# Performance work log

Hardware: AMD Instinct MI355X
Metric: run time of the kernel (lower is better)

The kernel has to match this reference:

```python
import jax, jax.numpy as jnp
import numpy as np

N, E = 20000, 320000
NODE_DIM, EDGE_DIM, EMB, HEADS, HIDDEN, OUT = 128, 16, 128, 4, 512, 64
NEG_SLOPE = 0.2


def _gatv2(x, src0, dst0, ea, Wl, bl, Wr, br, We, att, bias):
    """PyG GATv2Conv (concat=True, add_self_loops=True, fill_value='mean')."""
    n = x.shape[0]
    e = src0.shape[0]
    H, C = att.shape
    # self loops; self-loop edge_attr = mean of incoming edge_attr per node (0 if none)
    cnt = jax.ops.segment_sum(jnp.ones((e,), x.dtype), dst0, num_segments=n)
    loop_attr = jax.ops.segment_sum(ea, dst0, num_segments=n) / jnp.maximum(cnt, 1.0)[:, None]
    loops = jnp.arange(n, dtype=src0.dtype)
    src = jnp.concatenate([src0, loops])
    dst = jnp.concatenate([dst0, loops])
    ea_full = jnp.concatenate([ea, loop_attr], axis=0)
    xl = (x @ Wl + bl).reshape(n, H, C)   # source transform
    xr = (x @ Wr + br).reshape(n, H, C)   # target transform
    ef = (ea_full @ We).reshape(-1, H, C)  # edge transform (no bias in PyG)
    s = jax.nn.leaky_relu(xl[src] + xr[dst] + ef, NEG_SLOPE)  # [E', H, C]
    logits = jnp.einsum('ehc,hc->eh', s, att)
    # scatter-softmax over incoming edges of each dst node (stable)
    mx = jax.ops.segment_max(logits, dst, num_segments=n)
    num = jnp.exp(logits - mx[dst])
    den = jax.ops.segment_sum(num, dst, num_segments=n)
    alpha = num / (den[dst] + 1e-16)
    out = jax.ops.segment_sum(alpha[:, :, None] * xl[src], dst, num_segments=n)
    return out.reshape(n, H * C) + bias


def _lin(key, fan_in, fan_out, dt=jnp.float32):
    return jax.random.normal(key, (fan_in, fan_out), dt) * (1.0 / np.sqrt(fan_in))


def setup_inputs() -> dict:
    key = jax.random.key(0)
    ks = jax.random.split(key, 24)
    HC = HEADS * EMB
    inp = {
        'x': jax.random.normal(ks[0], (N, NODE_DIM), jnp.float32),
        'edge_index': jax.random.randint(ks[1], (2, E), 0, N, jnp.int64),
        'edge_attr': jax.random.normal(ks[2], (E, EDGE_DIM), jnp.float32),
        # GATv2 layer 1
        'Wl1': _lin(ks[3], NODE_DIM, HC), 'bl1': jnp.zeros((HC,), jnp.float32),
        'Wr1': _lin(ks[4], NODE_DIM, HC), 'br1': jnp.zeros((HC,), jnp.float32),
        'We1': _lin(ks[5], EDGE_DIM, HC),
        'att1': jax.random.normal(ks[6], (HEADS, EMB), jnp.float32) * (1.0 / np.sqrt(EMB)),
        'bias1': jnp.zeros((HC,), jnp.float32),
        # GATv2 layer 2
        'Wl2': _lin(ks[7], HC, HC), 'bl2': jnp.zeros((HC,), jnp.float32),
        'Wr2': _lin(ks[8], HC, HC), 'br2': jnp.zeros((HC,), jnp.float32),
        'We2': _lin(ks[9], EDGE_DIM, HC),
        'att2': jax.random.normal(ks[10], (HEADS, EMB), jnp.float32) * (1.0 / np.sqrt(EMB)),
        'bias2': jnp.zeros((HC,), jnp.float32),
        # decoder MLP
        'Wd1': _lin(ks[11], HC, HIDDEN), 'bd1': jnp.zeros((HIDDEN,), jnp.float32),
        'Wd2': _lin(ks[12], HIDDEN, OUT), 'bd2': jnp.zeros((OUT,), jnp.float32),
    }
    return inp


def reference(x, edge_index, edge_attr,
              Wl1, bl1, Wr1, br1, We1, att1, bias1,
              Wl2, bl2, Wr2, br2, We2, att2, bias2,
              Wd1, bd1, Wd2, bd2):
    src, dst = edge_index[0], edge_index[1]
    h = _gatv2(x, src, dst, edge_attr, Wl1, bl1, Wr1, br1, We1, att1, bias1)
    h = _gatv2(h, src, dst, edge_attr, Wl2, bl2, Wr2, br2, We2, att2, bias2)
    q = jax.nn.relu(h @ Wd1 + bd1) @ Wd2 + bd2
    return q
```

## Files before the change

### kernel.cpp

```cpp
#include <hip/hip_runtime.h>
#include <hip/hip_fp16.h>

typedef _Float16 half8 __attribute__((ext_vector_type(8)));
typedef _Float16 half2v __attribute__((ext_vector_type(2)));
typedef float f32x4 __attribute__((ext_vector_type(4)));

#if __has_builtin(__builtin_amdgcn_fdot2)
#define FDOT2(a, b, c) __builtin_amdgcn_fdot2((a), (b), (c), false)
#else
static __device__ __forceinline__ float FDOT2(half2v a, half2v b, float c) {
  return (float)a[0] * (float)b[0] + (float)a[1] * (float)b[1] + c;
}
#endif
#define H2(v8, p) ((half2v){(v8)[2 * (p)], (v8)[2 * (p) + 1]})

#define GLOAD_LDS16(gp, lp)                                                        \
  __builtin_amdgcn_global_load_lds(                                                \
      (const __attribute__((address_space(1))) void*)(gp),                         \
      (__attribute__((address_space(3))) void*)(lp), 16, 0, 0)

template <int CTRL>
__device__ __forceinline__ float dpp_add16(float x) {
  int y = __builtin_amdgcn_update_dpp(0, __float_as_int(x), CTRL, 0xf, 0xf, true);
  return x + __int_as_float(y);
}
__device__ __forceinline__ float rowsum16(float x) {
  x = dpp_add16<0x128>(x);
  x = dpp_add16<0x124>(x);
  x = dpp_add16<0x122>(x);
  x = dpp_add16<0x121>(x);
  return x;
}

__global__ void prep_kernel(const float* __restrict__ x, _Float16* __restrict__ x16, int nx,
                            const float* __restrict__ Wl1, const float* __restrict__ Wr1,
                            _Float16* __restrict__ WlrT1,
                            const float* __restrict__ Wl2, const float* __restrict__ Wr2,
                            _Float16* __restrict__ WlrT2,
                            const float* __restrict__ Wd1, _Float16* __restrict__ WdT1,
                            const float* __restrict__ Wd2, _Float16* __restrict__ WdT2,
                            const float* __restrict__ We1, _Float16* __restrict__ WeK1,
                            const float* __restrict__ We2, _Float16* __restrict__ WeK2,
                            const float* __restrict__ att1, _Float16* __restrict__ att16_1,
                            const float* __restrict__ att2, _Float16* __restrict__ att16_2,
                            const int* __restrict__ dst0, int* __restrict__ deg, int E) {
  int i = blockIdx.x * 256 + threadIdx.x;
  if (i < nx) { x16[i] = (_Float16)x[i]; return; }
  i -= nx;
  if (i < 1024 * 128) {
    int n = i >> 7, k = i & 127;
    float v = (n < 512) ? Wl1[(size_t)k * 512 + n] : Wr1[(size_t)k * 512 + (n - 512)];
    WlrT1[i] = (_Float16)v; return;
  }
  i -= 1024 * 128;
  if (i < 1024 * 512) {
    int n = i >> 9, k = i & 511;
    float v = (n < 512) ? Wl2[(size_t)k * 512 + n] : Wr2[(size_t)k * 512 + (n - 512)];
    WlrT2[i] = (_Float16)v; return;
  }
  i -= 1024 * 512;
  if (i < 512 * 512) { int n = i >> 9, k = i & 511; WdT1[i] = (_Float16)Wd1[(size_t)k * 512 + n]; return; }
  i -= 512 * 512;
  if (i < 64 * 512)  { int n = i >> 9, k = i & 511; WdT2[i] = (_Float16)Wd2[(size_t)k * 64 + n]; return; }
  i -= 64 * 512;
  if (i < 512 * 16)  { WeK1[i] = (_Float16)We1[i]; return; }
  i -= 512 * 16;
  if (i < 512 * 16)  { WeK2[i] = (_Float16)We2[i]; return; }
  i -= 512 * 16;
  if (i < 512)       { att16_1[i] = (_Float16)att1[i]; return; }
  i -= 512;
  if (i < 512)       { att16_2[i] = (_Float16)att2[i]; return; }
  i -= 512;
  if (i < E)         { atomicAdd(&deg[dst0[i]], 1); return; }
}

__global__ __launch_bounds__(1024) void scan_kernel(const int* __restrict__ deg, int* __restrict__ offs, int N) {
  __shared__ int part[1024];
  int t = threadIdx.x;
  int chunk = (N + 1023) / 1024;
  int b = t * chunk, e = min(b + chunk, N);
  int s = 0;
  for (int i = b; i < e; i++) s += deg[i] + 1;
  part[t] = s;
  __syncthreads();
  for (int off = 1; off < 1024; off <<= 1) {
    int v = (t >= off) ? part[t - off] : 0;
    __syncthreads();
    part[t] += v;
    __syncthreads();
  }
  int run = (t == 0) ? 0 : part[t - 1];
  for (int i = b; i < e; i++) { offs[i] = run; run += deg[i] + 1; }
  if (t == 1023) offs[N] = part[1023];
}

__global__ void csr_fill_kernel(const int* __restrict__ src0, const int* __restrict__ dst0,
                                const float* __restrict__ ea,
                                const int* __restrict__ offs, const int* __restrict__ deg,
                                int* __restrict__ cnt, int* __restrict__ csr_src,
                                _Float16* __restrict__ eas, int E, int N) {
  int i = blockIdx.x * 256 + threadIdx.x;
  if (i < 16) {
    csr_src[E + N + i] = 0;
#pragma unroll
    for (int k = 0; k < 16; k++) eas[(size_t)(E + N + i) * 16 + k] = (_Float16)0.f;
  }
  if (i < E) {
    int d = dst0[i];
    int p = offs[d] + atomicAdd(&cnt[d], 1);
    csr_src[p] = src0[i];
    const float* s = ea + (size_t)i * 16;
    half8 h0, h1;
#pragma unroll
    for (int k = 0; k < 8; k++) { h0[k] = (_Float16)s[k]; h1[k] = (_Float16)s[k + 8]; }
    *(half8*)(eas + (size_t)p * 16) = h0;
    *(half8*)(eas + (size_t)p * 16 + 8) = h1;
  } else if (i < E + N) {
    int v = i - E;
    csr_src[offs[v] + deg[v]] = v;
  }
}

__global__ void loop_attr_kernel(const int* __restrict__ offs, const int* __restrict__ deg,
                                 _Float16* __restrict__ eas, int N) {
  int i = blockIdx.x * 256 + threadIdx.x;
  if (i >= N * 16) return;
  int v = i >> 4, k = i & 15;
  int b = offs[v], dg = deg[v];
  float s = 0.f;
  for (int j = 0; j < dg; j++) s += (float)eas[((size_t)(b + j)) * 16 + k];
  eas[((size_t)(b + dg)) * 16 + k] = (_Float16)(s / fmaxf((float)dg, 1.0f));
}

template <bool RELU, bool OUT_F32>
__global__ __launch_bounds__(256) void gemm_f16(const _Float16* __restrict__ A,
                                                const _Float16* __restrict__ BT,
                                                const float* __restrict__ biasA,
                                                const float* __restrict__ biasB,
                                                void* __restrict__ C,
                                                int M, int K, int Nfull, int ldc) {
  __shared__ _Float16 As[128 * 32];
  __shared__ _Float16 Bs[128 * 32];
  int t = threadIdx.x;
  int m0 = blockIdx.x * 128;
  int n0 = blockIdx.y * 128;
  int l = t & 63, w = t >> 6;
  int wm = w & 1, wn = w >> 1;
  int lr = l & 15, lq = l >> 4;

  f32x4 acc[4][4];
#pragma unroll
  for (int i = 0; i < 4; i++)
#pragma unroll
    for (int j = 0; j < 4; j++) acc[i][j] = (f32x4){0.f, 0.f, 0.f, 0.f};

  int r0 = w * 32 + (l >> 2);
  int cb = (l & 3) * 8;
  const _Float16* Ap = A + (size_t)(m0 + r0) * K + cb;
  const _Float16* Bp = BT + (size_t)(n0 + r0) * K + cb;
  _Float16* AsW = As + w * 32 * 32;
  _Float16* BsW = Bs + w * 32 * 32;

  for (int kk = 0; kk < K; kk += 32) {
    GLOAD_LDS16(Ap, AsW);
    GLOAD_LDS16(Ap + (size_t)16 * K, AsW + 16 * 32);
    GLOAD_LDS16(Bp, BsW);
    GLOAD_LDS16(Bp + (size_t)16 * K, BsW + 16 * 32);
    Ap += 32; Bp += 32;
    __syncthreads();
    half8 af[4], bf[4];
#pragma unroll
    for (int mi = 0; mi < 4; mi++) af[mi] = *(const half8*)&As[(wm * 64 + mi * 16 + lr) * 32 + lq * 8];
#pragma unroll
    for (int ni = 0; ni < 4; ni++) bf[ni] = *(const half8*)&Bs[(wn * 64 + ni * 16 + lr) * 32 + lq * 8];
#pragma unroll
    for (int mi = 0; mi < 4; mi++)
#pragma unroll
      for (int ni = 0; ni < 4; ni++)
        acc[mi][ni] = __builtin_amdgcn_mfma_f32_16x16x32_f16(af[mi], bf[ni], acc[mi][ni], 0, 0, 0);
    __syncthreads();
  }

#pragma unroll
  for (int ni = 0; ni < 4; ni++) {
    int col = n0 + wn * 64 + ni * 16 + lr;
    if (col >= Nfull) continue;
    float bv = (col < 512) ? biasA[col] : biasB[col - 512];
#pragma unroll
    for (int mi = 0; mi < 4; mi++) {
#pragma unroll
      for (int r = 0; r < 4; r++) {
        int row = m0 + wm * 64 + mi * 16 + lq * 4 + r;
        if (row >= M) continue;
        float v = acc[mi][ni][r] + bv;
        if (RELU) v = fmaxf(v, 0.f);
        if (OUT_F32) ((float*)C)[(size_t)row * ldc + col] = v;
        else ((_Float16*)C)[(size_t)row * ldc + col] = (_Float16)v;
      }
    }
  }
}


__device__ __forceinline__ void upd(float p, half8 xs, float& m, float& den, float acc[8]) {
  float mn = fmaxf(m, p);
  float sc = __expf(m - mn);
  float al = __expf(p - mn);
  den = den * sc + al;
#pragma unroll
  for (int jj = 0; jj < 8; jj++) acc[jj] = acc[jj] * sc + al * (float)xs[jj];
  m = mn;
}

__global__ __launch_bounds__(256) void gat_fused_kernel(
    const _Float16* __restrict__ xlr,
    const int* __restrict__ csr_src, const int* __restrict__ offs,
    const _Float16* __restrict__ eas,
    const _Float16* __restrict__ WeK,
    const _Float16* __restrict__ att16,
    const float* __restrict__ bias,
    _Float16* __restrict__ hout, int N) {
  __shared__ _Float16 WeL[16 * 512];
  int t = threadIdx.x;
  int l = t & 63;
  int w = t >> 6;
  int h = l >> 4;
  int c0 = l * 8;

  {
    const _Float16* gW = WeK + w * 512 + l * 8;
    _Float16* lW = WeL + w * 512;
#pragma unroll
    for (int p = 0; p < 4; p++) GLOAD_LDS16(gW + p * 2048, lW + p * 2048);
  }
  __syncthreads();

  half8 attv = *(const half8*)(att16 + h * 128 + (l & 15) * 8);
  const half2v lk = {(_Float16)0.2f, (_Float16)0.2f};

  int wid = blockIdx.x * 4 + w;
  int nw = gridDim.x * 4;

  for (int v0 = wid; v0 < N; v0 += nw) {
    int v = __builtin_amdgcn_readfirstlane(v0);
    int b = offs[v], e2 = offs[v + 1];
    half8 xrv = *(const half8*)(xlr + (size_t)v * 1024 + 512 + c0);

    int s0 = csr_src[b], s1 = csr_src[b + 1], s2 = csr_src[b + 2], s3 = csr_src[b + 3];
    half8 xs0 = *(const half8*)(xlr + (size_t)s0 * 1024 + c0);
    half8 xs1 = *(const half8*)(xlr + (size_t)s1 * 1024 + c0);
    half8 xs2 = *(const half8*)(xlr + (size_t)s2 * 1024 + c0);
    half8 xs3 = *(const half8*)(xlr + (size_t)s3 * 1024 + c0);
    half8 a00 = *(const half8*)(eas + (size_t)b * 16);
    half8 a01 = *(const half8*)(eas + (size_t)b * 16 + 8);
    half8 a10 = *(const half8*)(eas + (size_t)(b + 1) * 16);
    half8 a11 = *(const half8*)(eas + (size_t)(b + 1) * 16 + 8);
    half8 a20 = *(const half8*)(eas + (size_t)(b + 2) * 16);
    half8 a21 = *(const half8*)(eas + (size_t)(b + 2) * 16 + 8);
    half8 a30 = *(const half8*)(eas + (size_t)(b + 3) * 16);
    half8 a31 = *(const half8*)(eas + (size_t)(b + 3) * 16 + 8);
    int t0 = csr_src[b + 4], t1 = csr_src[b + 5], t2 = csr_src[b + 6], t3 = csr_src[b + 7];

    float m = -1e30f, den = 0.f;
    float acc[8];
#pragma unroll
    for (int j = 0; j < 8; j++) acc[j] = 0.f;

    for (int j = b; j < e2; j += 4) {
      half8 nx0 = *(const half8*)(xlr + (size_t)t0 * 1024 + c0);
      half8 nx1 = *(const half8*)(xlr + (size_t)t1 * 1024 + c0);
      half8 nx2 = *(const half8*)(xlr + (size_t)t2 * 1024 + c0);
      half8 nx3 = *(const half8*)(xlr + (size_t)t3 * 1024 + c0);
      half8 n00 = *(const half8*)(eas + (size_t)(j + 4) * 16);
      half8 n01 = *(const half8*)(eas + (size_t)(j + 4) * 16 + 8);
      half8 n10 = *(const half8*)(eas + (size_t)(j + 5) * 16);
      half8 n11 = *(const half8*)(eas + (size_t)(j + 5) * 16 + 8);
      half8 n20 = *(const half8*)(eas + (size_t)(j + 6) * 16);
      half8 n21 = *(const half8*)(eas + (size_t)(j + 6) * 16 + 8);
      half8 n30 = *(const half8*)(eas + (size_t)(j + 7) * 16);
      half8 n31 = *(const half8*)(eas + (size_t)(j + 7) * 16 + 8);
      int u0 = csr_src[j + 8], u1 = csr_src[j + 9], u2 = csr_src[j + 10], u3 = csr_src[j + 11];

      half2v e0[4], e1[4], e2v[4], e3[4];
#pragma unroll
      for (int p = 0; p < 4; p++) {
        e0[p] = (half2v){0, 0}; e1[p] = (half2v){0, 0};
        e2v[p] = (half2v){0, 0}; e3[p] = (half2v){0, 0};
      }
#pragma unroll
      for (int k = 0; k < 16; k++) {
        half8 wr = *(const half8*)(WeL + k * 512 + c0);
        _Float16 q0 = (k < 8) ? a00[k] : a01[k - 8];
        _Float16 q1 = (k < 8) ? a10[k] : a11[k - 8];
        _Float16 q2 = (k < 8) ? a20[k] : a21[k - 8];
        _Float16 q3 = (k < 8) ? a30[k] : a31[k - 8];
        half2v k0 = {q0, q0}, k1 = {q1, q1}, k2 = {q2, q2}, k3 = {q3, q3};
#pragma unroll
        for (int p = 0; p < 4; p++) {
          half2v wp = H2(wr, p);
          e0[p] += k0 * wp;
          e1[p] += k1 * wp;
          e2v[p] += k2 * wp;
          e3[p] += k3 * wp;
        }
      }
      float p0 = 0.f, p1 = 0.f, p2 = 0.f, p3 = 0.f;
#pragma unroll
      for (int p = 0; p < 4; p++) {
        half2v xrp = H2(xrv, p);
        half2v ap = H2(attv, p);
        half2v v0 = H2(xs0, p) + xrp + e0[p];
        half2v v1 = H2(xs1, p) + xrp + e1[p];
        half2v v2 = H2(xs2, p) + xrp + e2v[p];
        half2v v3 = H2(xs3, p) + xrp + e3[p];
        v0 = __builtin_elementwise_max(v0, v0 * lk);
        v1 = __builtin_elementwise_max(v1, v1 * lk);
        v2 = __builtin_elementwise_max(v2, v2 * lk);
        v3 = __builtin_elementwise_max(v3, v3 * lk);
        p0 = FDOT2(v0, ap, p0);
        p1 = FDOT2(v1, ap, p1);
        p2 = FDOT2(v2, ap, p2);
        p3 = FDOT2(v3, ap, p3);
      }
      p0 = rowsum16(p0); p1 = rowsum16(p1); p2 = rowsum16(p2); p3 = rowsum16(p3);

      upd(p0, xs0, m, den, acc);
      if (j + 1 < e2) upd(p1, xs1, m, den, acc);
      if (j + 2 < e2) upd(p2, xs2, m, den, acc);
      if (j + 3 < e2) upd(p3, xs3, m, den, acc);

      xs0 = nx0; xs1 = nx1; xs2 = nx2; xs3 = nx3;
      a00 = n00; a01 = n01; a10 = n10; a11 = n11;
      a20 = n20; a21 = n21; a30 = n30; a31 = n31;
      t0 = u0; t1 = u1; t2 = u2; t3 = u3;
    }
    float rd = 1.f / (den + 1e-16f);
    half8 o;
#pragma unroll
    for (int jj = 0; jj < 8; jj++) o[jj] = (_Float16)(fmaf(acc[jj], rd, bias[c0 + jj]));
    *(half8*)(hout + (size_t)v * 512 + c0) = o;
  }
}


extern "C" void kernel_launch(void* const* d_in, const int* in_sizes, int n_in,
                              void* d_out, int out_size, void* d_ws, size_t ws_size,
                              hipStream_t stream) {
  (void)n_in; (void)out_size; (void)ws_size;
  const float* x    = (const float*)d_in[0];
  const int*   ei   = (const int*)d_in[1];
  const float* ea   = (const float*)d_in[2];
  const float* Wl1  = (const float*)d_in[3];
  const float* bl1  = (const float*)d_in[4];
  const float* Wr1  = (const float*)d_in[5];
  const float* br1  = (const float*)d_in[6];
  const float* We1  = (const float*)d_in[7];
  const float* att1 = (const float*)d_in[8];
  const float* bias1= (const float*)d_in[9];
  const float* Wl2  = (const float*)d_in[10];
  const float* bl2  = (const float*)d_in[11];
  const float* Wr2  = (const float*)d_in[12];
  const float* br2  = (const float*)d_in[13];
  const float* We2  = (const float*)d_in[14];
  const float* att2 = (const float*)d_in[15];
  const float* bias2= (const float*)d_in[16];
  const float* Wd1  = (const float*)d_in[17];
  const float* bd1  = (const float*)d_in[18];
  const float* Wd2  = (const float*)d_in[19];
  const float* bd2  = (const float*)d_in[20];

  const int N = in_sizes[0] / 128;
  const int E = in_sizes[1] / 2;
  const int EP = E + N;
  const int Npad = (N + 127) & ~127;
  const int* src0 = ei;
  const int* dst0 = ei + E;

  char* ws = (char*)d_ws;
  size_t off = 0;
  auto alloc = [&](size_t bytes) -> void* {
    void* p = ws + off;
    off += (bytes + 255) & ~(size_t)255;
    return p;
  };

  int*   deg    = (int*)alloc((size_t)N * 8);
  int*   cnt    = deg + N;
  int*   offs   = (int*)alloc(((size_t)N + 1) * 4);
  int*   csr_src= (int*)alloc(((size_t)EP + 16) * 4);
  _Float16* eas = (_Float16*)alloc(((size_t)EP + 16) * 16 * 2);
  _Float16* x16   = (_Float16*)alloc((size_t)Npad * 128 * 2);
  _Float16* xlr16 = (_Float16*)alloc((size_t)Npad * 1024 * 2);
  _Float16* h16   = (_Float16*)alloc((size_t)Npad * 512 * 2);
  _Float16* WlrT1 = (_Float16*)alloc(1024 * 128 * 2);
  _Float16* WlrT2 = (_Float16*)alloc(1024 * 512 * 2);
  _Float16* WdT1  = (_Float16*)alloc(512 * 512 * 2);
  _Float16* WdT2  = (_Float16*)alloc(128 * 512 * 2);
  _Float16* WeK1  = (_Float16*)alloc(16 * 512 * 2);
  _Float16* WeK2  = (_Float16*)alloc(16 * 512 * 2);
  _Float16* att16_1 = (_Float16*)alloc(512 * 2);
  _Float16* att16_2 = (_Float16*)alloc(512 * 2);
  _Float16* t16   = xlr16;

  hipMemsetAsync(deg, 0, (size_t)N * 8, stream);

  int nx = N * 128;
  int prep_base = nx + 1024 * 128 + 1024 * 512 + 512 * 512 + 64 * 512
                + 512 * 16 + 512 * 16 + 512 + 512;
  int prep_total = prep_base + E;
  prep_kernel<<<(prep_total + 255) / 256, 256, 0, stream>>>(
      x, x16, nx, Wl1, Wr1, WlrT1, Wl2, Wr2, WlrT2,
      Wd1, WdT1, Wd2, WdT2, We1, WeK1, We2, WeK2,
      att1, att16_1, att2, att16_2, dst0, deg, E);

  int g;
  scan_kernel<<<1, 1024, 0, stream>>>(deg, offs, N);
  g = (EP + 255) / 256;
  csr_fill_kernel<<<g, 256, 0, stream>>>(src0, dst0, ea, offs, deg, cnt, csr_src, eas, E, N);
  g = (N * 16 + 255) / 256;
  loop_attr_kernel<<<g, 256, 0, stream>>>(offs, deg, eas, N);

  dim3 gb(256);
  dim3 ggm((N + 127) / 128, 8);
  dim3 ggd((N + 127) / 128, 4);
  dim3 ggo((N + 127) / 128, 1);

  const int FGRID = 2048;

  gemm_f16<false, false><<<ggm, gb, 0, stream>>>(x16, WlrT1, bl1, br1, xlr16, N, 128, 1024, 1024);
  gat_fused_kernel<<<FGRID, 256, 0, stream>>>(xlr16, csr_src, offs, eas, WeK1, att16_1, bias1, h16, N);

  gemm_f16<false, false><<<ggm, gb, 0, stream>>>(h16, WlrT2, bl2, br2, xlr16, N, 512, 1024, 1024);
  gat_fused_kernel<<<FGRID, 256, 0, stream>>>(xlr16, csr_src, offs, eas, WeK2, att16_2, bias2, h16, N);

  gemm_f16<true, false><<<ggd, gb, 0, stream>>>(h16, WdT1, bd1, bd1, t16, N, 512, 512, 512);
  gemm_f16<false, true><<<ggo, gb, 0, stream>>>(t16, WdT2, bd2, bd2, d_out, N, 512, 64, 64);
}
```

Before: 534.1 us.

## Compute per-edge edge-feature projections with MFMA into swizzled LDS tiles

Inside the fused GAT kernel, the per-edge edge_attr @ We projection moves from packed-half FMAs per edge to 16x16x16 MFMA instructions. Each wave computes a chunk of 16 edges by 512 channels into a per-wave swizzled LDS buffer, and the attention loop reads those projections back from LDS. We is reordered in prep to suit the MFMA A-fragment layout, and padding is extended to cover chunk overreads. Separately, the loop-attr mean kernel uses one wave per node with shuffle reduction. The cost is 64KB of extra LDS per block, which may reduce occupancy, and wasted MFMA work for nodes with low degree.

```diff
diff --git a/kernel.cpp b/kernel.cpp
--- a/kernel.cpp
+++ b/kernel.cpp
@@ -2,6 +2,7 @@
 #include <hip/hip_fp16.h>
 
 typedef _Float16 half8 __attribute__((ext_vector_type(8)));
+typedef _Float16 half4 __attribute__((ext_vector_type(4)));
 typedef _Float16 half2v __attribute__((ext_vector_type(2)));
 typedef float f32x4 __attribute__((ext_vector_type(4)));
 
@@ -39,8 +40,8 @@
                             _Float16* __restrict__ WlrT2,
                             const float* __restrict__ Wd1, _Float16* __restrict__ WdT1,
                             const float* __restrict__ Wd2, _Float16* __restrict__ WdT2,
-                            const float* __restrict__ We1, _Float16* __restrict__ WeK1,
-                            const float* __restrict__ We2, _Float16* __restrict__ WeK2,
+                            const float* __restrict__ We1, _Float16* __restrict__ WeF1,
+                            const float* __restrict__ We2, _Float16* __restrict__ WeF2,
                             const float* __restrict__ att1, _Float16* __restrict__ att16_1,
                             const float* __restrict__ att2, _Float16* __restrict__ att16_2,
                             const int* __restrict__ dst0, int* __restrict__ deg, int E) {
@@ -63,9 +64,15 @@
   i -= 512 * 512;
   if (i < 64 * 512)  { int n = i >> 9, k = i & 511; WdT2[i] = (_Float16)Wd2[(size_t)k * 64 + n]; return; }
   i -= 64 * 512;
-  if (i < 512 * 16)  { WeK1[i] = (_Float16)We1[i]; return; }
+  if (i < 512 * 16) {
+    int k = i & 15, c = (i >> 4) & 15, g = i >> 8;
+    WeF1[i] = (_Float16)We1[(size_t)k * 512 + g * 16 + c]; return;
+  }
   i -= 512 * 16;
-  if (i < 512 * 16)  { WeK2[i] = (_Float16)We2[i]; return; }
+  if (i < 512 * 16) {
+    int k = i & 15, c = (i >> 4) & 15, g = i >> 8;
+    WeF2[i] = (_Float16)We2[(size_t)k * 512 + g * 16 + c]; return;
+  }
   i -= 512 * 16;
   if (i < 512)       { att16_1[i] = (_Float16)att1[i]; return; }
   i -= 512;
@@ -100,8 +107,8 @@
                                 int* __restrict__ cnt, int* __restrict__ csr_src,
                                 _Float16* __restrict__ eas, int E, int N) {
   int i = blockIdx.x * 256 + threadIdx.x;
-  if (i < 16) {
-    csr_src[E + N + i] = 0;
+  if (i < 64) {
+    if (i < 16) csr_src[E + N + i] = 0;
 #pragma unroll
     for (int k = 0; k < 16; k++) eas[(size_t)(E + N + i) * 16 + k] = (_Float16)0.f;
   }
@@ -123,13 +130,17 @@
 
 __global__ void loop_attr_kernel(const int* __restrict__ offs, const int* __restrict__ deg,
                                  _Float16* __restrict__ eas, int N) {
-  int i = blockIdx.x * 256 + threadIdx.x;
-  if (i >= N * 16) return;
-  int v = i >> 4, k = i & 15;
-  int b = offs[v], dg = deg[v];
+  int wid = (blockIdx.x * 256 + threadIdx.x) >> 6;
+  int l = threadIdx.x & 63;
+  if (wid >= N) return;
+  int b = offs[wid], dg = deg[wid];
+  int k = l & 15, r = l >> 4;
   float s = 0.f;
-  for (int j = 0; j < dg; j++) s += (float)eas[((size_t)(b + j)) * 16 + k];
-  eas[((size_t)(b + dg)) * 16 + k] = (_Float16)(s / fmaxf((float)dg, 1.0f));
+  for (int j = r; j < dg; j += 4)
+    s += (float)eas[(size_t)(b + j) * 16 + k];
+  s += __shfl_xor(s, 16, 64);
+  s += __shfl_xor(s, 32, 64);
+  if (r == 0) eas[(size_t)(b + dg) * 16 + k] = (_Float16)(s / fmaxf((float)dg, 1.0f));
 }
 
 template <bool RELU, bool OUT_F32>
@@ -216,26 +227,29 @@
     const _Float16* __restrict__ xlr,
     const int* __restrict__ csr_src, const int* __restrict__ offs,
     const _Float16* __restrict__ eas,
-    const _Float16* __restrict__ WeK,
+    const _Float16* __restrict__ WeF,
     const _Float16* __restrict__ att16,
     const float* __restrict__ bias,
     _Float16* __restrict__ hout, int N) {
-  __shared__ _Float16 WeL[16 * 512];
+  __shared__ _Float16 WeFL[16 * 512];
+  __shared__ _Float16 EFs[4][16 * 512];
   int t = threadIdx.x;
   int l = t & 63;
   int w = t >> 6;
   int h = l >> 4;
   int c0 = l * 8;
+  int lr = l & 15, lq = l >> 4;
 
   {
-    const _Float16* gW = WeK + w * 512 + l * 8;
-    _Float16* lW = WeL + w * 512;
+    const _Float16* gW = WeF + w * 512 + l * 8;
+    _Float16* lW = WeFL + w * 512;
 #pragma unroll
     for (int p = 0; p < 4; p++) GLOAD_LDS16(gW + p * 2048, lW + p * 2048);
   }
   __syncthreads();
 
-  half8 attv = *(const half8*)(att16 + h * 128 + (l & 15) * 8);
+  _Float16* EFw = &EFs[w][0];
+  half8 attv = *(const half8*)(att16 + h * 128 + lr * 8);
   const half2v lk = {(_Float16)0.2f, (_Float16)0.2f};
 
   int wid = blockIdx.x * 4 + w;
@@ -251,88 +265,67 @@
     half8 xs1 = *(const half8*)(xlr + (size_t)s1 * 1024 + c0);
     half8 xs2 = *(const half8*)(xlr + (size_t)s2 * 1024 + c0);
     half8 xs3 = *(const half8*)(xlr + (size_t)s3 * 1024 + c0);
-    half8 a00 = *(const half8*)(eas + (size_t)b * 16);
-    half8 a01 = *(const half8*)(eas + (size_t)b * 16 + 8);
-    half8 a10 = *(const half8*)(eas + (size_t)(b + 1) * 16);
-    half8 a11 = *(const half8*)(eas + (size_t)(b + 1) * 16 + 8);
-    half8 a20 = *(const half8*)(eas + (size_t)(b + 2) * 16);
-    half8 a21 = *(const half8*)(eas + (size_t)(b + 2) * 16 + 8);
-    half8 a30 = *(const half8*)(eas + (size_t)(b + 3) * 16);
-    half8 a31 = *(const half8*)(eas + (size_t)(b + 3) * 16 + 8);
     int t0 = csr_src[b + 4], t1 = csr_src[b + 5], t2 = csr_src[b + 6], t3 = csr_src[b + 7];
+    half4 bfrag = *(const half4*)(eas + (size_t)(b + lr) * 16 + lq * 4);
 
     float m = -1e30f, den = 0.f;
     float acc[8];
 #pragma unroll
     for (int j = 0; j < 8; j++) acc[j] = 0.f;
 
-    for (int j = b; j < e2; j += 4) {
-      half8 nx0 = *(const half8*)(xlr + (size_t)t0 * 1024 + c0);
-      half8 nx1 = *(const half8*)(xlr + (size_t)t1 * 1024 + c0);
-      half8 nx2 = *(const half8*)(xlr + (size_t)t2 * 1024 + c0);
-      half8 nx3 = *(const half8*)(xlr + (size_t)t3 * 1024 + c0);
-      half8 n00 = *(const half8*)(eas + (size_t)(j + 4) * 16);
-      half8 n01 = *(const half8*)(eas + (size_t)(j + 4) * 16 + 8);
-      half8 n10 = *(const half8*)(eas + (size_t)(j + 5) * 16);
-      half8 n11 = *(const half8*)(eas + (size_t)(j + 5) * 16 + 8);
-      half8 n20 = *(const half8*)(eas + (size_t)(j + 6) * 16);
-      half8 n21 = *(const half8*)(eas + (size_t)(j + 6) * 16 + 8);
-      half8 n30 = *(const half8*)(eas + (size_t)(j + 7) * 16);
-      half8 n31 = *(const half8*)(eas + (size_t)(j + 7) * 16 + 8);
-      int u0 = csr_src[j + 8], u1 = csr_src[j + 9], u2 = csr_src[j + 10], u3 = csr_src[j + 11];
-
-      half2v e0[4], e1[4], e2v[4], e3[4];
-#pragma unroll
-      for (int p = 0; p < 4; p++) {
-        e0[p] = (half2v){0, 0}; e1[p] = (half2v){0, 0};
-        e2v[p] = (half2v){0, 0}; e3[p] = (half2v){0, 0};
+    for (int cs = b; cs < e2; cs += 16) {
+#pragma unroll
+      for (int g = 0; g < 32; g++) {
+        half4 af = *(const half4*)(WeFL + g * 256 + lr * 16 + lq * 4);
+        f32x4 d = __builtin_amdgcn_mfma_f32_16x16x16f16(af, bfrag, (f32x4){0.f, 0.f, 0.f, 0.f}, 0, 0, 0);
+        half4 hd = {(_Float16)d[0], (_Float16)d[1], (_Float16)d[2], (_Float16)d[3]};
+        int hi = (lr * 512 + g * 16 + lq * 4) ^ ((lr & 7) << 3);
+        *(half4*)(EFw + hi) = hd;
       }
-#pragma unroll
-      for (int k = 0; k < 16; k++) {
-        half8 wr = *(const half8*)(WeL + k * 512 + c0);
-        _Float16 q0 = (k < 8) ? a00[k] : a01[k - 8];
-        _Float16 q1 = (k < 8) ? a10[k] : a11[k - 8];
-        _Float16 q2 = (k < 8) ? a20[k] : a21[k - 8];
-        _Float16 q3 = (k < 8) ? a30[k] : a31[k - 8];
-        half2v k0 = {q0, q0}, k1 = {q1, q1}, k2 = {q2, q2}, k3 = {q3, q3};
+      bfrag = *(const half4*)(eas + (size_t)(cs + 16 + lr) * 16 + lq * 4);
+
+      int cse = min(cs + 16, e2);
+      for (int j = cs; j < cse; j += 4) {
+        half8 nx0 = *(const half8*)(xlr + (size_t)t0 * 1024 + c0);
+        half8 nx1 = *(const half8*)(xlr + (size_t)t1 * 1024 + c0);
+        half8 nx2 = *(const half8*)(xlr + (size_t)t2 * 1024 + c0);
+        half8 nx3 = *(const half8*)(xlr + (size_t)t3 * 1024 + c0);
+        int u0 = csr_src[j + 8], u1 = csr_src[j + 9], u2 = csr_src[j + 10], u3 = csr_src[j + 11];
+
+        int si = j - cs;
+        half8 ef0 = *(const half8*)(EFw + (((si    ) * 512 + l * 8) ^ (((si    ) & 7) << 3)));
+        half8 ef1 = *(const half8*)(EFw + (((si + 1) * 512 + l * 8) ^ (((si + 1) & 7) << 3)));
+        half8 ef2 = *(const half8*)(EFw + (((si + 2) * 512 + l * 8) ^ (((si + 2) & 7) << 3)));
+        half8 ef3 = *(const half8*)(EFw + (((si + 3) * 512 + l * 8) ^ (((si + 3) & 7) << 3)));
+
+        float p0 = 0.f, p1 = 0.f, p2 = 0.f, p3 = 0.f;
 #pragma unroll
         for (int p = 0; p < 4; p++) {
-          half2v wp = H2(wr, p);
-          e0[p] += k0 * wp;
-          e1[p] += k1 * wp;
-          e2v[p] += k2 * wp;
-          e3[p] += k3 * wp;
+          half2v xrp = H2(xrv, p);
+          half2v ap = H2(attv, p);
+          half2v v0v = H2(xs0, p) + xrp + H2(ef0, p);
+          half2v v1v = H2(xs1, p) + xrp + H2(ef1, p);
+          half2v v2v = H2(xs2, p) + xrp + H2(ef2, p);
+          half2v v3v = H2(xs3, p) + xrp + H2(ef3, p);
+          v0v = __builtin_elementwise_max(v0v, v0v * lk);
+          v1v = __builtin_elementwise_max(v1v, v1v * lk);
+          v2v = __builtin_elementwise_max(v2v, v2v * lk);
+          v3v = __builtin_elementwise_max(v3v, v3v * lk);
+          p0 = FDOT2(v0v, ap, p0);
+          p1 = FDOT2(v1v, ap, p1);
+          p2 = FDOT2(v2v, ap, p2);
+          p3 = FDOT2(v3v, ap, p3);
         }
+        p0 = rowsum16(p0); p1 = rowsum16(p1); p2 = rowsum16(p2); p3 = rowsum16(p3);
+
+        upd(p0, xs0, m, den, acc);
+        if (j + 1 < e2) upd(p1, xs1, m, den, acc);
+        if (j + 2 < e2) upd(p2, xs2, m, den, acc);
+        if (j + 3 < e2) upd(p3, xs3, m, den, acc);
+
+        xs0 = nx0; xs1 = nx1; xs2 = nx2; xs3 = nx3;
+        t0 = u0; t1 = u1; t2 = u2; t3 = u3;
       }
-      float p0 = 0.f, p1 = 0.f, p2 = 0.f, p3 = 0.f;
-#pragma unroll
-      for (int p = 0; p < 4; p++) {
-        half2v xrp = H2(xrv, p);
-        half2v ap = H2(attv, p);
-        half2v v0 = H2(xs0, p) + xrp + e0[p];
-        half2v v1 = H2(xs1, p) + xrp + e1[p];
-        half2v v2 = H2(xs2, p) + xrp + e2v[p];
-        half2v v3 = H2(xs3, p) + xrp + e3[p];
-        v0 = __builtin_elementwise_max(v0, v0 * lk);
-        v1 = __builtin_elementwise_max(v1, v1 * lk);
-        v2 = __builtin_elementwise_max(v2, v2 * lk);
-        v3 = __builtin_elementwise_max(v3, v3 * lk);
-        p0 = FDOT2(v0, ap, p0);
-        p1 = FDOT2(v1, ap, p1);
-        p2 = FDOT2(v2, ap, p2);
-        p3 = FDOT2(v3, ap, p3);
-      }
-      p0 = rowsum16(p0); p1 = rowsum16(p1); p2 = rowsum16(p2); p3 = rowsum16(p3);
-
-      upd(p0, xs0, m, den, acc);
-      if (j + 1 < e2) upd(p1, xs1, m, den, acc);
-      if (j + 2 < e2) upd(p2, xs2, m, den, acc);
-      if (j + 3 < e2) upd(p3, xs3, m, den, acc);
-
-      xs0 = nx0; xs1 = nx1; xs2 = nx2; xs3 = nx3;
-      a00 = n00; a01 = n01; a10 = n10; a11 = n11;
-      a20 = n20; a21 = n21; a30 = n30; a31 = n31;
-      t0 = u0; t1 = u1; t2 = u2; t3 = u3;
     }
     float rd = 1.f / (den + 1e-16f);
     half8 o;
@@ -388,7 +381,7 @@
   int*   cnt    = deg + N;
   int*   offs   = (int*)alloc(((size_t)N + 1) * 4);
   int*   csr_src= (int*)alloc(((size_t)EP + 16) * 4);
-  _Float16* eas = (_Float16*)alloc(((size_t)EP + 16) * 16 * 2);
+  _Float16* eas = (_Float16*)alloc(((size_t)EP + 64) * 16 * 2);
   _Float16* x16   = (_Float16*)alloc((size_t)Npad * 128 * 2);
   _Float16* xlr16 = (_Float16*)alloc((size_t)Npad * 1024 * 2);
   _Float16* h16   = (_Float16*)alloc((size_t)Npad * 512 * 2);
@@ -396,8 +389,8 @@
   _Float16* WlrT2 = (_Float16*)alloc(1024 * 512 * 2);
   _Float16* WdT1  = (_Float16*)alloc(512 * 512 * 2);
   _Float16* WdT2  = (_Float16*)alloc(128 * 512 * 2);
-  _Float16* WeK1  = (_Float16*)alloc(16 * 512 * 2);
-  _Float16* WeK2  = (_Float16*)alloc(16 * 512 * 2);
+  _Float16* WeF1  = (_Float16*)alloc(16 * 512 * 2);
+  _Float16* WeF2  = (_Float16*)alloc(16 * 512 * 2);
   _Float16* att16_1 = (_Float16*)alloc(512 * 2);
   _Float16* att16_2 = (_Float16*)alloc(512 * 2);
   _Float16* t16   = xlr16;
@@ -410,14 +403,14 @@
   int prep_total = prep_base + E;
   prep_kernel<<<(prep_total + 255) / 256, 256, 0, stream>>>(
       x, x16, nx, Wl1, Wr1, WlrT1, Wl2, Wr2, WlrT2,
-      Wd1, WdT1, Wd2, WdT2, We1, WeK1, We2, WeK2,
+      Wd1, WdT1, Wd2, WdT2, We1, WeF1, We2, WeF2,
       att1, att16_1, att2, att16_2, dst0, deg, E);
 
   int g;
   scan_kernel<<<1, 1024, 0, stream>>>(deg, offs, N);
   g = (EP + 255) / 256;
   csr_fill_kernel<<<g, 256, 0, stream>>>(src0, dst0, ea, offs, deg, cnt, csr_src, eas, E, N);
-  g = (N * 16 + 255) / 256;
+  g = (N * 64 + 255) / 256;
   loop_attr_kernel<<<g, 256, 0, stream>>>(offs, deg, eas, N);
 
   dim3 gb(256);
@@ -428,10 +421,10 @@
   const int FGRID = 2048;
 
   gemm_f16<false, false><<<ggm, gb, 0, stream>>>(x16, WlrT1, bl1, br1, xlr16, N, 128, 1024, 1024);
-  gat_fused_kernel<<<FGRID, 256, 0, stream>>>(xlr16, csr_src, offs, eas, WeK1, att16_1, bias1, h16, N);
+  gat_fused_kernel<<<FGRID, 256, 0, stream>>>(xlr16, csr_src, offs, eas, WeF1, att16_1, bias1, h16, N);
 
   gemm_f16<false, false><<<ggm, gb, 0, stream>>>(h16, WlrT2, bl2, br2, xlr16, N, 512, 1024, 1024);
-  gat_fused_kernel<<<FGRID, 256, 0, stream>>>(xlr16, csr_src, offs, eas, WeK2, att16_2, bias2, h16, N);
+  gat_fused_kernel<<<FGRID, 256, 0, stream>>>(xlr16, csr_src, offs, eas, WeF2, att16_2, bias2, h16, N);
 
   gemm_f16<true, false><<<ggd, gb, 0, stream>>>(h16, WdT1, bd1, bd1, t16, N, 512, 512, 512);
   gemm_f16<false, true><<<ggo, gb, 0, stream>>>(t16, WdT2, bd2, bd2, d_out, N, 512, 64, 64);
```

After: 509.1 us. 1.05x faster.
